# Kernel optimization log

Measured on AMD Instinct MI355X. Metric: run time of the kernel, lower is better.

Reference implementation:

```python
import jax, jax.numpy as jnp
import numpy as np

EPS = 1e-6

def _det3(m):
    return (m[..., 0, 0] * m[..., 1, 1] * m[..., 2, 2]
            + m[..., 0, 1] * m[..., 1, 2] * m[..., 2, 0]
            + m[..., 1, 0] * m[..., 2, 1] * m[..., 0, 2]
            - m[..., 2, 0] * m[..., 1, 1] * m[..., 0, 2]
            - m[..., 0, 0] * m[..., 2, 1] * m[..., 1, 2]
            - m[..., 1, 0] * m[..., 0, 1] * m[..., 2, 2])

def _inv3(m):
    a, b, c = m[..., 0, 0], m[..., 0, 1], m[..., 0, 2]
    d, e, f = m[..., 1, 0], m[..., 1, 1], m[..., 1, 2]
    g, h, i = m[..., 2, 0], m[..., 2, 1], m[..., 2, 2]
    adj = jnp.stack([
        jnp.stack([e * i - f * h, c * h - b * i, b * f - c * e], -1),
        jnp.stack([f * g - d * i, a * i - c * g, c * d - a * f], -1),
        jnp.stack([d * h - e * g, b * g - a * h, a * e - b * d], -1)], -2)
    return adj / _det3(m)[..., None, None]

def setup_inputs() -> dict:
    key = jax.random.key(0)
    ks = jax.random.split(key, 12)
    N, B, DH = 100000, 2048, 256
    idx = jnp.sort(jnp.concatenate([jnp.arange(B, dtype=jnp.int32),
                                    jax.random.randint(ks[0], (N - B,), 0, B, dtype=jnp.int32)]))
    return {
        "t": jax.random.uniform(ks[1], (B, 1), jnp.float32, 0.01, 0.99),
        "h": jax.random.normal(ks[2], (N, DH), jnp.float32),
        "pos": jax.random.normal(ks[3], (N, 3), jnp.float32),
        "eps_h": jax.random.normal(ks[4], (N, DH), jnp.float32),
        "eps_pos": jax.random.normal(ks[5], (N, 3), jnp.float32),
        "gparam_h": jax.random.normal(ks[6], (1, 1), jnp.float32),
        "gparam_pos": jax.random.normal(ks[7], (1, 1), jnp.float32),
        "W_mu": jax.random.normal(ks[8], (DH, DH), jnp.float32) / np.sqrt(DH),
        "W_r1": jax.random.normal(ks[9], (DH, 2 * DH), jnp.float32) / np.sqrt(DH),
        "W_r2": jax.random.normal(ks[10], (2 * DH, DH), jnp.float32) / np.sqrt(2 * DH),
        "index": idx,
        "num_graphs": B,
    }


def _forward(t, h, pos, eps_h, eps_pos, gparam_h, gparam_pos, W_mu, W_r1, W_r2, index, B):
    eye = jnp.eye(3, dtype=h.dtype)
    seg_sum = lambda x: jax.ops.segment_sum(x, index, num_segments=B)
    counts = seg_sum(jnp.ones((index.shape[0],), h.dtype))  # [B]

    def scatter_center(x):  # x - per-graph mean, gathered back
        mean = seg_sum(x) / counts[:, None]
        return x - mean[index]

    # volatility g(t): per-graph, gathered to nodes
    g_h = (0.1 + jax.nn.softplus(gparam_h) * t)[index]      # [N,1]
    g_pos = (0.1 + jax.nn.softplus(gparam_pos) * t)[index]  # [N,1]

    def f_net(t_, hh, pp):  # surrogate forward transformation f
        tn = t_[index]                                      # [N,1]
        mu_h = (hh @ W_mu) * (1.0 - tn)
        sigma_h = 0.1 + 0.9 * tn                            # [N,1]
        mu_pos = pp * (1.0 - tn)
        nrm = pp / (jnp.linalg.norm(pp, axis=-1, keepdims=True) + EPS)
        a = (0.2 + 0.8 * tn)[..., None]                     # [N,1,1]
        b = (0.1 * tn)[..., None]
        U = a * eye + b * (nrm[:, :, None] * nrm[:, None, :])  # [N,3,3]
        return mu_h, sigma_h, mu_pos, U

    def z_pos_fn(mu, U, eps):
        return mu + scatter_center(jnp.einsum('nij,nj->ni', U, eps))

    def score_pos_fn(eps, U, inv_U=None, C=None):
        if inv_U is None or C is None:
            inv_U = _inv3(U)
            inv_V = _inv3(seg_sum(inv_U))
            C = inv_V[index] @ (inv_U - eye)
        y = jnp.einsum('nji,nj->ni', inv_U, eps)
        ybar = seg_sum(y)
        c = jnp.einsum('nji,nj->ni', C, ybar[index])
        return scatter_center(c - y)  # zero_cog_score=True

    def solve_pos_fn(U, prel):
        inv_U = _inv3(U)
        inv_V = _inv3(seg_sum(inv_U))
        C = inv_V[index] @ (inv_U - eye)
        c = seg_sum(jnp.einsum('nij,nj->ni', C, prel))[index]
        eps = jnp.einsum('nij,nj->ni', inv_U, prel - c)
        return eps, inv_U, C

    bdrift = lambda dz, score, g: dz - 0.5 * g ** 2 * score

    # ---- target backward drift (time_derivative via jvp over t) ----
    (mu_h, sig_h, mu_p, U), (dmu_h, dsig_h, dmu_p, dU) = jax.jvp(
        lambda tt: f_net(tt, h, pos), (t,), (jnp.ones_like(t),))
    z_h = mu_h + sig_h * eps_h
    dz_h = dmu_h + dsig_h * eps_h
    z_p = z_pos_fn(mu_p, U, eps_pos)
    dz_p = z_pos_fn(dmu_p, dU, eps_pos)
    tgt_h = bdrift(dz_h, -eps_h / sig_h, g_h)
    tgt_p = bdrift(dz_p, score_pos_fn(eps_pos, U), g_pos)

    # ---- approximate backward drift ('x0' parameterization) ----
    h_r = jnp.tanh(z_h @ W_r1) @ W_r2   # reconstructor r
    pos_r = z_p * 0.9
    (mu_h2, sig_h2, mu_p2, U2), (dmu_h2, dsig_h2, dmu_p2, dU2) = jax.jvp(
        lambda tt: f_net(tt, h_r, pos_r), (t,), (jnp.ones_like(t),))
    eps_h2 = (z_h - mu_h2) / sig_h2
    eps_p2, inv_U2, C2 = solve_pos_fn(U2, z_p - mu_p2)
    dz_h2 = dmu_h2 + dsig_h2 * eps_h2
    dz_p2 = z_pos_fn(dmu_p2, dU2, eps_p2)
    apx_h = bdrift(dz_h2, -eps_h2 / sig_h2, g_h)
    apx_p = bdrift(dz_p2, score_pos_fn(eps_p2, U2, inv_U2, C2), g_pos)

    # ---- 'simple' loss: mse(approx/g, target/g) ----
    loss_h = jnp.mean(((apx_h - tgt_h) / g_h) ** 2)
    loss_p = jnp.mean(((apx_p - tgt_p) / g_pos) ** 2)
    return loss_h, loss_p


def reference(t, h, pos, eps_h, eps_pos, gparam_h, gparam_pos, W_mu, W_r1, W_r2, index, num_graphs):
    return _forward(t, h, pos, eps_h, eps_pos, gparam_h, gparam_pos, W_mu, W_r1, W_r2, index, num_graphs)
```

## Files before the change

kernel.cpp:

```cpp
#include <hip/hip_runtime.h>
#include <math.h>

#define NTHREADS 256
#define EPSC 1e-6f
#define NPL 3

typedef short bf16x8 __attribute__((ext_vector_type(8)));
typedef float f32x4  __attribute__((ext_vector_type(4)));

#define GLDS(srcp, dstp) __builtin_amdgcn_global_load_lds( \
    (const __attribute__((address_space(1))) void*)(srcp), \
    (__attribute__((address_space(3))) void*)(dstp), 16, 0, 0)

__device__ __forceinline__ ushort f2bf(float x) {
  union { float f; unsigned u; } v; v.f = x;
  unsigned r = v.u + 0x7FFFu + ((v.u >> 16) & 1u);
  return (ushort)(r >> 16);
}
__device__ __forceinline__ float bf2f(ushort x) {
  union { unsigned u; float f; } v; v.u = ((unsigned)x) << 16;
  return v.f;
}
__device__ __forceinline__ float tanh_fast(float x) {
  float xc = fminf(fmaxf(x, -15.f), 15.f);
  float e = __expf(2.f * xc);
  return (e - 1.f) / (e + 1.f);
}

__device__ __forceinline__ void inv3x3(const float m[9], float o[9]) {
  float a=m[0],b=m[1],c=m[2],d=m[3],e=m[4],f=m[5],g=m[6],h=m[7],i=m[8];
  float det = a*e*i + b*f*g + d*h*c - g*e*c - a*h*f - d*b*i;
  float r = 1.0f/det;
  o[0]=(e*i-f*h)*r; o[1]=(c*h-b*i)*r; o[2]=(b*f-c*e)*r;
  o[3]=(f*g-d*i)*r; o[4]=(a*i-c*g)*r; o[5]=(c*d-a*f)*r;
  o[6]=(d*h-e*g)*r; o[7]=(b*g-a*h)*r; o[8]=(a*e-b*d)*r;
}

__device__ __forceinline__ float wred(float v) {
#pragma unroll
  for (int o = 32; o > 0; o >>= 1) v += __shfl_xor(v, o, 64);
  return v;
}

__device__ void pos_graph(
    int b, int lane, int N,
    const float* __restrict__ pos, const float* __restrict__ epsp,
    const int* __restrict__ index, const float* __restrict__ t,
    const float* __restrict__ gpp, double* __restrict__ lossp)
{
  int lo = 0, hi = N;
  while (lo < hi) { int mid = (lo + hi) >> 1; if (index[mid] < b) lo = mid + 1; else hi = mid; }
  const int start = lo;
  hi = N;
  while (lo < hi) { int mid = (lo + hi) >> 1; if (index[mid] < b + 1) lo = mid + 1; else hi = mid; }
  const int end = lo;
  const int cnt = end - start;
  const float fn = (float)cnt, rc = 1.0f / fn;

  const float tn  = t[b];
  const float a1  = 0.2f + 0.8f*tn, b1 = 0.1f*tn;
  const float omt = 1.0f - tn;
  const float sp  = log1pf(expf(gpp[0]));
  const float gp  = 0.1f + sp*tn;
  const float hg  = 0.5f*gp*gp;
  const float rgp = 1.0f/gp;
  const float pscale = 1.0f - 0.9f*omt;

  float iU[NPL][9], yv[NPL][3], wv[NPL][3], dwv[NPL][3], pv[NPL][3];
  float Vs[9] = {0}, wb[3] = {0}, dwb[3] = {0}, yb[3] = {0};
#pragma unroll
  for (int k = 0; k < NPL; ++k) {
    const int n = start + k*64 + lane;
    if (n < end) {
      const float px = pos[3*(size_t)n+0], py = pos[3*(size_t)n+1], pz = pos[3*(size_t)n+2];
      const float ex = epsp[3*(size_t)n+0], ey = epsp[3*(size_t)n+1], ez = epsp[3*(size_t)n+2];
      pv[k][0]=px; pv[k][1]=py; pv[k][2]=pz;
      const float pn = sqrtf(px*px+py*py+pz*pz) + EPSC;
      const float nx = px/pn, ny = py/pn, nz = pz/pn;
      const float nd = nx*ex + ny*ey + nz*ez;
      wv[k][0]=a1*ex + b1*nd*nx; wv[k][1]=a1*ey + b1*nd*ny; wv[k][2]=a1*ez + b1*nd*nz;
      dwv[k][0]=0.8f*ex + 0.1f*nd*nx; dwv[k][1]=0.8f*ey + 0.1f*nd*ny; dwv[k][2]=0.8f*ez + 0.1f*nd*nz;
      const float U[9] = { a1 + b1*nx*nx, b1*nx*ny,      b1*nx*nz,
                           b1*ny*nx,      a1 + b1*ny*ny, b1*ny*nz,
                           b1*nz*nx,      b1*nz*ny,      a1 + b1*nz*nz };
      inv3x3(U, iU[k]);
      yv[k][0] = iU[k][0]*ex + iU[k][3]*ey + iU[k][6]*ez;
      yv[k][1] = iU[k][1]*ex + iU[k][4]*ey + iU[k][7]*ez;
      yv[k][2] = iU[k][2]*ex + iU[k][5]*ey + iU[k][8]*ez;
#pragma unroll
      for (int j = 0; j < 9; ++j) Vs[j] += iU[k][j];
#pragma unroll
      for (int j = 0; j < 3; ++j) { wb[j]+=wv[k][j]; dwb[j]+=dwv[k][j]; yb[j]+=yv[k][j]; }
    }
  }
#pragma unroll
  for (int j = 0; j < 9; ++j) Vs[j] = wred(Vs[j]);
#pragma unroll
  for (int j = 0; j < 3; ++j) { wb[j]=wred(wb[j]); dwb[j]=wred(dwb[j]); yb[j]=wred(yb[j]); }

  float iV[9]; inv3x3(Vs, iV);
  float wm[3], dwm[3], u1[3], s1m[3];
#pragma unroll
  for (int i = 0; i < 3; ++i) { wm[i] = wb[i]*rc; dwm[i] = dwb[i]*rc; }
#pragma unroll
  for (int i = 0; i < 3; ++i) u1[i] = iV[0*3+i]*yb[0] + iV[1*3+i]*yb[1] + iV[2*3+i]*yb[2];
#pragma unroll
  for (int i = 0; i < 3; ++i) {
    const float csy = Vs[0*3+i]*u1[0] + Vs[1*3+i]*u1[1] + Vs[2*3+i]*u1[2] - fn*u1[i];
    s1m[i] = (csy - yb[i]) * rc;
  }

  float tg[NPL][3], zp[NPL][3], iU2[NPL][9], qv[NPL][3];
  float Vs2[9] = {0}, qs[3] = {0}, ps[3] = {0};
#pragma unroll
  for (int k = 0; k < NPL; ++k) {
    const int n = start + k*64 + lane;
    if (n < end) {
#pragma unroll
      for (int i = 0; i < 3; ++i) {
        const float c1 = iU[k][0*3+i]*u1[0] + iU[k][1*3+i]*u1[1] + iU[k][2*3+i]*u1[2] - u1[i];
        const float score1 = c1 - yv[k][i] - s1m[i];
        tg[k][i] = -pv[k][i] + dwv[k][i] - dwm[i] - hg*score1;
        zp[k][i] = pv[k][i]*omt + wv[k][i] - wm[i];
      }
      const float rx = 0.9f*zp[k][0], ry = 0.9f*zp[k][1], rz = 0.9f*zp[k][2];
      const float rn = sqrtf(rx*rx+ry*ry+rz*rz) + EPSC;
      const float nx = rx/rn, ny = ry/rn, nz = rz/rn;
      const float U2[9] = { a1 + b1*nx*nx, b1*nx*ny,      b1*nx*nz,
                            b1*ny*nx,      a1 + b1*ny*ny, b1*ny*nz,
                            b1*nz*nx,      b1*nz*ny,      a1 + b1*nz*nz };
      inv3x3(U2, iU2[k]);
      float prel[3];
#pragma unroll
      for (int i = 0; i < 3; ++i) prel[i] = zp[k][i]*pscale;
#pragma unroll
      for (int i = 0; i < 3; ++i)
        qv[k][i] = iU2[k][i*3+0]*prel[0] + iU2[k][i*3+1]*prel[1] + iU2[k][i*3+2]*prel[2];
#pragma unroll
      for (int j = 0; j < 9; ++j) Vs2[j] += iU2[k][j];
#pragma unroll
      for (int j = 0; j < 3; ++j) { qs[j] += qv[k][j]; ps[j] += prel[j]; }
    }
  }
#pragma unroll
  for (int j = 0; j < 9; ++j) Vs2[j] = wred(Vs2[j]);
#pragma unroll
  for (int j = 0; j < 3; ++j) { qs[j] = wred(qs[j]); ps[j] = wred(ps[j]); }

  float iV2[9]; inv3x3(Vs2, iV2);
  float cb2[3];
#pragma unroll
  for (int i = 0; i < 3; ++i)
    cb2[i] = iV2[i*3+0]*(qs[0]-ps[0]) + iV2[i*3+1]*(qs[1]-ps[1]) + iV2[i*3+2]*(qs[2]-ps[2]);

  float y2v[NPL][3], dw2v[NPL][3];
  float yb2[3] = {0}, dwb2[3] = {0};
#pragma unroll
  for (int k = 0; k < NPL; ++k) {
    const int n = start + k*64 + lane;
    if (n < end) {
      float e[3];
#pragma unroll
      for (int i = 0; i < 3; ++i)
        e[i] = qv[k][i] - (iU2[k][i*3+0]*cb2[0] + iU2[k][i*3+1]*cb2[1] + iU2[k][i*3+2]*cb2[2]);
#pragma unroll
      for (int i = 0; i < 3; ++i)
        y2v[k][i] = iU2[k][0*3+i]*e[0] + iU2[k][1*3+i]*e[1] + iU2[k][2*3+i]*e[2];
      const float rx = 0.9f*zp[k][0], ry = 0.9f*zp[k][1], rz = 0.9f*zp[k][2];
      const float rn = sqrtf(rx*rx+ry*ry+rz*rz) + EPSC;
      const float nx = rx/rn, ny = ry/rn, nz = rz/rn;
      const float nd = nx*e[0] + ny*e[1] + nz*e[2];
      dw2v[k][0] = 0.8f*e[0] + 0.1f*nd*nx;
      dw2v[k][1] = 0.8f*e[1] + 0.1f*nd*ny;
      dw2v[k][2] = 0.8f*e[2] + 0.1f*nd*nz;
#pragma unroll
      for (int j = 0; j < 3; ++j) { yb2[j] += y2v[k][j]; dwb2[j] += dw2v[k][j]; }
    }
  }
#pragma unroll
  for (int j = 0; j < 3; ++j) { yb2[j] = wred(yb2[j]); dwb2[j] = wred(dwb2[j]); }

  float u2[3], s2m[3], dw2m[3];
#pragma unroll
  for (int i = 0; i < 3; ++i) u2[i] = iV2[0*3+i]*yb2[0] + iV2[1*3+i]*yb2[1] + iV2[2*3+i]*yb2[2];
#pragma unroll
  for (int i = 0; i < 3; ++i) {
    const float csy = Vs2[0*3+i]*u2[0] + Vs2[1*3+i]*u2[1] + Vs2[2*3+i]*u2[2] - fn*u2[i];
    s2m[i] = (csy - yb2[i]) * rc;
    dw2m[i] = dwb2[i] * rc;
  }

  float acc = 0.0f;
#pragma unroll
  for (int k = 0; k < NPL; ++k) {
    const int n = start + k*64 + lane;
    if (n < end) {
#pragma unroll
      for (int i = 0; i < 3; ++i) {
        const float c2 = iU2[k][0*3+i]*u2[0] + iU2[k][1*3+i]*u2[1] + iU2[k][2*3+i]*u2[2] - u2[i];
        const float score2 = c2 - y2v[k][i] - s2m[i];
        const float dz2 = -0.9f*zp[k][i] + dw2v[k][i] - dw2m[i];
        const float apx = dz2 - hg*score2;
        const float d = (apx - tg[k][i]) * rgp;
        acc += d*d;
      }
    }
  }
  acc = wred(acc);
  if (lane == 0) atomicAdd(lossp, (double)acc);
}

__global__ __launch_bounds__(NTHREADS) void prep_all(
    const float4* __restrict__ h, ushort4* __restrict__ hb, int n4h,
    const float4* __restrict__ wr2, ushort4* __restrict__ wr2b, int n4w,
    const float* __restrict__ wmu, ushort* __restrict__ wmut,
    const float* __restrict__ wr1, ushort* __restrict__ wr1t)
{
  __shared__ float ts[32][33];
  const int bid = blockIdx.x;
  if (bid < 2048) {
    for (int i = bid*NTHREADS + threadIdx.x; i < n4h; i += 2048*NTHREADS) {
      float4 v = h[i];
      hb[i] = make_ushort4(f2bf(v.x), f2bf(v.y), f2bf(v.z), f2bf(v.w));
    }
  } else if (bid < 2176) {
    for (int i = (bid-2048)*NTHREADS + threadIdx.x; i < n4w; i += 128*NTHREADS) {
      float4 v = wr2[i];
      wr2b[i] = make_ushort4(f2bf(v.x), f2bf(v.y), f2bf(v.z), f2bf(v.w));
    }
  } else if (bid < 2240) {
    const int vb = bid - 2176;
    const int nb = (vb & 7)*32, kb = (vb >> 3)*32;
    const int tx = threadIdx.x & 31, ty = threadIdx.x >> 5;
#pragma unroll
    for (int r = 0; r < 4; ++r)
      ts[ty + r*8][tx] = wmu[(size_t)(kb + ty + r*8)*256 + nb + tx];
    __syncthreads();
#pragma unroll
    for (int r = 0; r < 4; ++r)
      wmut[(size_t)(nb + ty + r*8)*256 + kb + tx] = f2bf(ts[tx][ty + r*8]);
  } else {
    const int vb = bid - 2240;
    const int nb = (vb & 15)*32, kb = (vb >> 4)*32;
    const int tx = threadIdx.x & 31, ty = threadIdx.x >> 5;
#pragma unroll
    for (int r = 0; r < 4; ++r)
      ts[ty + r*8][tx] = wr1[(size_t)(kb + ty + r*8)*512 + nb + tx];
    __syncthreads();
#pragma unroll
    for (int r = 0; r < 4; ++r)
      wr1t[(size_t)(nb + ty + r*8)*256 + kb + tx] = f2bf(ts[tx][ty + r*8]);
  }
}

__global__ __launch_bounds__(256) void gemm_wcomb(
    const ushort* __restrict__ A, const ushort* __restrict__ Bt,
    int K, int Nn, int Mvalid, ushort* __restrict__ OutB)
{
  __shared__ __align__(16) ushort As[128*32];
  __shared__ __align__(16) ushort Bs[128*32];
  const int tid = threadIdx.x;
  const int row0 = blockIdx.y*128, col0 = blockIdx.x*128;
  const int wave = tid >> 6, lane = tid & 63;
  const int wm = (wave & 1)*64, wn = (wave >> 1)*64;
  const int lm = lane & 15, lq = lane >> 4;

  f32x4 acc[4][4];
#pragma unroll
  for (int i = 0; i < 4; ++i)
#pragma unroll
    for (int j = 0; j < 4; ++j) { acc[i][j][0]=0.f; acc[i][j][1]=0.f; acc[i][j][2]=0.f; acc[i][j][3]=0.f; }

  const int c0 = tid, c1 = tid + 256;
  const int r0a = c0 >> 2, k0a = (c0 & 3) << 3;
  const int r1a = c1 >> 2, k1a = (c1 & 3) << 3;

  for (int k0 = 0; k0 < K; k0 += 32) {
    __syncthreads();
    GLDS(A  + (size_t)(row0 + r0a)*K + k0 + k0a, As + c0*8);
    GLDS(A  + (size_t)(row0 + r1a)*K + k0 + k1a, As + c1*8);
    GLDS(Bt + (size_t)(col0 + r0a)*K + k0 + k0a, Bs + c0*8);
    GLDS(Bt + (size_t)(col0 + r1a)*K + k0 + k1a, Bs + c1*8);
    __syncthreads();

    bf16x8 af[4], bfr[4];
#pragma unroll
    for (int i = 0; i < 4; ++i)
      af[i] = *(const bf16x8*)&As[(wm + i*16 + lm)*32 + lq*8];
#pragma unroll
    for (int j = 0; j < 4; ++j)
      bfr[j] = *(const bf16x8*)&Bs[(wn + j*16 + lm)*32 + lq*8];
#pragma unroll
    for (int i = 0; i < 4; ++i)
#pragma unroll
      for (int j = 0; j < 4; ++j)
        acc[i][j] = __builtin_amdgcn_mfma_f32_16x16x32_bf16(af[i], bfr[j], acc[i][j], 0, 0, 0);
  }

#pragma unroll
  for (int i = 0; i < 4; ++i) {
#pragma unroll
    for (int reg = 0; reg < 4; ++reg) {
      const int r = row0 + wm + i*16 + lq*4 + reg;
#pragma unroll
      for (int j = 0; j < 4; ++j) {
        const int cc = col0 + wn + j*16 + lm;
        OutB[(size_t)cc*Mvalid + r] = f2bf(-acc[i][j][reg]);
      }
    }
  }
}

__global__ __launch_bounds__(256, 3) void fused_main(
    int PB, int Bg,
    const float* __restrict__ pos, const float* __restrict__ epsp,
    const float* __restrict__ gpp, double* __restrict__ lossp,
    const ushort* __restrict__ hb, const ushort* __restrict__ wmut,
    const ushort* __restrict__ wr1t, const ushort* __restrict__ wct,
    const float* __restrict__ eps, const int* __restrict__ index,
    const float* __restrict__ t, const float* __restrict__ gph,
    int N, double* __restrict__ lossAcc)
{
  __shared__ __align__(16) ushort zs[64*256];
  __shared__ __align__(16) ushort t1s[64*128];

  const int wave = threadIdx.x >> 6, lane = threadIdx.x & 63;

  if (blockIdx.x < PB) {
    const int b = blockIdx.x*4 + wave;
    if (b < Bg) pos_graph(b, lane, N, pos, epsp, index, t, gpp, lossp);
    return;
  }

  const int row0 = (blockIdx.x - PB) * 64;
  const int lm = lane & 15, lq = lane >> 4;
  const int wn  = wave * 64;
  const int wn2 = wave * 32;

  f32x4 acc[4][4];
#pragma unroll
  for (int i = 0; i < 4; ++i)
#pragma unroll
    for (int j = 0; j < 4; ++j) { acc[i][j][0]=0.f; acc[i][j][1]=0.f; acc[i][j][2]=0.f; acc[i][j][3]=0.f; }

#pragma unroll
  for (int k = 0; k < 8; ++k) {
    bf16x8 a_[4], b_[4];
#pragma unroll
    for (int i = 0; i < 4; ++i)
      a_[i] = *(const bf16x8*)(hb + (size_t)(row0 + i*16 + lm)*256 + k*32 + lq*8);
#pragma unroll
    for (int j = 0; j < 4; ++j)
      b_[j] = *(const bf16x8*)(wmut + (size_t)(wn + j*16 + lm)*256 + k*32 + lq*8);
#pragma unroll
    for (int i = 0; i < 4; ++i)
#pragma unroll
      for (int j = 0; j < 4; ++j)
        acc[i][j] = __builtin_amdgcn_mfma_f32_16x16x32_bf16(a_[i], b_[j], acc[i][j], 0, 0, 0);
  }

#pragma unroll
  for (int i = 0; i < 4; ++i) {
#pragma unroll
    for (int reg = 0; reg < 4; ++reg) {
      const int rb = i*16 + lq*4 + reg;
      const int r = row0 + rb;
      const int rcl = (r < N) ? r : (N - 1);
      const float tn = t[index[rcl]];
      const float s0 = 1.0f - tn, s1 = 0.1f + 0.9f*tn;
#pragma unroll
      for (int j = 0; j < 4; ++j) {
        const int cc = wn + j*16 + lm;
        const float z = acc[i][j][reg]*s0 + s1*eps[(size_t)rcl*256 + cc];
        zs[rb*256 + (cc ^ ((rb & 7) << 3))] = f2bf(z);
      }
    }
  }
  __syncthreads();

  for (int c2 = 0; c2 < 4; ++c2) {
    f32x4 acct[4][2];
#pragma unroll
    for (int i = 0; i < 4; ++i)
#pragma unroll
      for (int j = 0; j < 2; ++j) { acct[i][j][0]=0.f; acct[i][j][1]=0.f; acct[i][j][2]=0.f; acct[i][j][3]=0.f; }

#pragma unroll
    for (int k = 0; k < 8; ++k) {
      bf16x8 az[4], b_[2];
#pragma unroll
      for (int i = 0; i < 4; ++i) {
        const int r = i*16 + lm;
        const int c = k*32 + lq*8;
        az[i] = *(const bf16x8*)&zs[r*256 + (c ^ ((r & 7) << 3))];
      }
#pragma unroll
      for (int j = 0; j < 2; ++j)
        b_[j] = *(const bf16x8*)(wr1t + (size_t)(c2*128 + wn2 + j*16 + lm)*256 + k*32 + lq*8);
#pragma unroll
      for (int i = 0; i < 4; ++i)
#pragma unroll
        for (int j = 0; j < 2; ++j)
          acct[i][j] = __builtin_amdgcn_mfma_f32_16x16x32_bf16(az[i], b_[j], acct[i][j], 0, 0, 0);
    }

    bf16x8 pb[4];
#pragma unroll
    for (int j = 0; j < 4; ++j)
      pb[j] = *(const bf16x8*)(wct + (size_t)(wn + j*16 + lm)*512 + c2*128 + lq*8);

    __syncthreads();
#pragma unroll
    for (int i = 0; i < 4; ++i)
#pragma unroll
      for (int j = 0; j < 2; ++j)
#pragma unroll
        for (int reg = 0; reg < 4; ++reg) {
          const int rb = i*16 + lq*4 + reg;
          const int c = wn2 + j*16 + lm;
          t1s[rb*128 + (c ^ ((rb & 7) << 3))] = f2bf(tanh_fast(acct[i][j][reg]));
        }
    __syncthreads();

#pragma unroll
    for (int k = 0; k < 4; ++k) {
      bf16x8 at[4], b_[4];
#pragma unroll
      for (int i = 0; i < 4; ++i) {
        const int r = i*16 + lm;
        const int c = k*32 + lq*8;
        at[i] = *(const bf16x8*)&t1s[r*128 + (c ^ ((r & 7) << 3))];
      }
      if (k == 0) {
#pragma unroll
        for (int j = 0; j < 4; ++j) b_[j] = pb[j];
      } else {
#pragma unroll
        for (int j = 0; j < 4; ++j)
          b_[j] = *(const bf16x8*)(wct + (size_t)(wn + j*16 + lm)*512 + c2*128 + k*32 + lq*8);
      }
#pragma unroll
      for (int i = 0; i < 4; ++i)
#pragma unroll
        for (int j = 0; j < 4; ++j)
          acc[i][j] = __builtin_amdgcn_mfma_f32_16x16x32_bf16(at[i], b_[j], acc[i][j], 0, 0, 0);
    }
  }

  const float sp = log1pf(expf(gph[0]));
  float local = 0.f;
#pragma unroll
  for (int i = 0; i < 4; ++i) {
#pragma unroll
    for (int reg = 0; reg < 4; ++reg) {
      const int r = row0 + i*16 + lq*4 + reg;
      if (r < N) {
        const float tn = t[index[r]];
        const float gh  = 0.1f + sp*tn;
        const float sig = 0.1f + 0.9f*tn;
        const float fac = 1.0f + (0.9f + 0.5f*gh*gh/sig)*(1.0f - tn)/sig;
        const float sc  = fac/gh;
#pragma unroll
        for (int j = 0; j < 4; ++j) {
          const float d = acc[i][j][reg] * sc;
          local += d*d;
        }
      }
    }
  }
  double dv = (double)local;
#pragma unroll
  for (int off = 32; off > 0; off >>= 1) dv += __shfl_down(dv, off, 64);
  if (lane == 0) atomicAdd(lossAcc, dv);
}

__global__ void finalize_kernel(const double* lossh, const double* lossp,
                                float* out, int N, int DH)
{
  if (threadIdx.x == 0) {
    out[0] = (float)(lossh[0] / ((double)N * (double)DH));
    out[1] = (float)(lossp[0] / ((double)N * 3.0));
  }
}

extern "C" void kernel_launch(void* const* d_in, const int* in_sizes, int n_in,
                              void* d_out, int out_size, void* d_ws, size_t ws_size,
                              hipStream_t stream) {
  const float* t      = (const float*)d_in[0];
  const float* h      = (const float*)d_in[1];
  const float* pos    = (const float*)d_in[2];
  const float* eps_h  = (const float*)d_in[3];
  const float* eps_p  = (const float*)d_in[4];
  const float* gph    = (const float*)d_in[5];
  const float* gpp    = (const float*)d_in[6];
  const float* W_mu   = (const float*)d_in[7];
  const float* W_r1   = (const float*)d_in[8];
  const float* W_r2   = (const float*)d_in[9];
  const int*   index  = (const int*)d_in[10];
  const int B = in_sizes[0];
  const int N = in_sizes[10];
  const int DH = 256, DH2 = 512;
  const int NPAD = 100352;

  char* ws = (char*)d_ws;
  size_t off = 0;
  auto alloc = [&](size_t nbytes) { size_t o = off; off += (nbytes + 255) & ~(size_t)255; return o; };

  size_t o_loss = alloc(16);
  size_t o_hb   = alloc((size_t)NPAD*DH*2);
  size_t o_wmut = alloc((size_t)DH*DH*2);
  size_t o_wr1t = alloc((size_t)DH2*DH*2);
  size_t o_wr2b = alloc((size_t)DH2*DH*2);
  size_t o_wct  = alloc((size_t)DH*DH2*2);

  hipMemsetAsync(ws + o_loss, 0, 16, stream);

  double* lossh = (double*)(ws + o_loss);
  double* lossp = lossh + 1;
  ushort* hb   = (ushort*)(ws + o_hb);
  ushort* wmut = (ushort*)(ws + o_wmut);
  ushort* wr1t = (ushort*)(ws + o_wr1t);
  ushort* wr2b = (ushort*)(ws + o_wr2b);
  ushort* wct  = (ushort*)(ws + o_wct);

  prep_all<<<2368, NTHREADS, 0, stream>>>(
      (const float4*)h, (ushort4*)hb, N*DH/4,
      (const float4*)W_r2, (ushort4*)wr2b, DH2*DH/4,
      W_mu, wmut, W_r1, wr1t);

  gemm_wcomb<<<dim3(DH/128, DH2/128), 256, 0, stream>>>(
      wr2b, wmut, DH, DH, DH2, wct);

  const int PB = (B + 3) / 4;
  const int HB = (N + 63) / 64;
  fused_main<<<PB + HB, 256, 0, stream>>>(
      PB, B, pos, eps_p, gpp, lossp,
      hb, wmut, wr1t, wct, eps_h, index, t, gph, N, lossh);

  finalize_kernel<<<1, 64, 0, stream>>>(lossh, lossp, (float*)d_out, N, DH);
}
```

Baseline: 545.5 us.

## Fuse h bf16 conversion into main GEMM and split pos branch into own kernel

Drops the separate pass that converted all of h to a bf16 workspace copy. The main h kernel now reads fp32 h directly and packs it to bf16 in registers before the MFMA, which removes a full write and re-read of the converted matrix. The per-graph position branch moves out of the fused kernel into its own launch with one 64-thread block per graph. The h kernel's occupancy hint drops from 3 to 2 blocks per CU and the wct prefetch is removed, trading a bigger fp32 load per tile for less total memory traffic.

Result: faster. 489.2 us (-10.3%).

```diff
diff --git a/kernel.cpp b/kernel.cpp
--- a/kernel.cpp
+++ b/kernel.cpp
@@ -20,6 +20,12 @@
 __device__ __forceinline__ float bf2f(ushort x) {
   union { unsigned u; float f; } v; v.u = ((unsigned)x) << 16;
   return v.f;
+}
+__device__ __forceinline__ bf16x8 pack8(float4 a, float4 b) {
+  bf16x8 r;
+  r[0]=(short)f2bf(a.x); r[1]=(short)f2bf(a.y); r[2]=(short)f2bf(a.z); r[3]=(short)f2bf(a.w);
+  r[4]=(short)f2bf(b.x); r[5]=(short)f2bf(b.y); r[6]=(short)f2bf(b.z); r[7]=(short)f2bf(b.w);
+  return r;
 }
 __device__ __forceinline__ float tanh_fast(float x) {
   float xc = fminf(fmaxf(x, -15.f), 15.f);
@@ -42,12 +48,14 @@
   return v;
 }
 
-__device__ void pos_graph(
-    int b, int lane, int N,
-    const float* __restrict__ pos, const float* __restrict__ epsp,
+__global__ __launch_bounds__(64) void pos_branch_v4b(
+    int N, const float* __restrict__ pos, const float* __restrict__ epsp,
     const int* __restrict__ index, const float* __restrict__ t,
     const float* __restrict__ gpp, double* __restrict__ lossp)
 {
+  const int b = blockIdx.x;
+  const int lane = threadIdx.x;
+
   int lo = 0, hi = N;
   while (lo < hi) { int mid = (lo + hi) >> 1; if (index[mid] < b) lo = mid + 1; else hi = mid; }
   const int start = lo;
@@ -210,26 +218,21 @@
   if (lane == 0) atomicAdd(lossp, (double)acc);
 }
 
-__global__ __launch_bounds__(NTHREADS) void prep_all(
-    const float4* __restrict__ h, ushort4* __restrict__ hb, int n4h,
+__global__ __launch_bounds__(NTHREADS) void prep_weights_v4b(
     const float4* __restrict__ wr2, ushort4* __restrict__ wr2b, int n4w,
     const float* __restrict__ wmu, ushort* __restrict__ wmut,
     const float* __restrict__ wr1, ushort* __restrict__ wr1t)
 {
   __shared__ float ts[32][33];
   const int bid = blockIdx.x;
-  if (bid < 2048) {
-    for (int i = bid*NTHREADS + threadIdx.x; i < n4h; i += 2048*NTHREADS) {
-      float4 v = h[i];
-      hb[i] = make_ushort4(f2bf(v.x), f2bf(v.y), f2bf(v.z), f2bf(v.w));
-    }
-  } else if (bid < 2176) {
-    for (int i = (bid-2048)*NTHREADS + threadIdx.x; i < n4w; i += 128*NTHREADS) {
+  if (bid < 128) {
+    const int i = bid*NTHREADS + threadIdx.x;
+    if (i < n4w) {
       float4 v = wr2[i];
       wr2b[i] = make_ushort4(f2bf(v.x), f2bf(v.y), f2bf(v.z), f2bf(v.w));
     }
-  } else if (bid < 2240) {
-    const int vb = bid - 2176;
+  } else if (bid < 192) {
+    const int vb = bid - 128;
     const int nb = (vb & 7)*32, kb = (vb >> 3)*32;
     const int tx = threadIdx.x & 31, ty = threadIdx.x >> 5;
 #pragma unroll
@@ -240,7 +243,7 @@
     for (int r = 0; r < 4; ++r)
       wmut[(size_t)(nb + ty + r*8)*256 + kb + tx] = f2bf(ts[tx][ty + r*8]);
   } else {
-    const int vb = bid - 2240;
+    const int vb = bid - 192;
     const int nb = (vb & 15)*32, kb = (vb >> 4)*32;
     const int tx = threadIdx.x & 31, ty = threadIdx.x >> 5;
 #pragma unroll
@@ -253,7 +256,7 @@
   }
 }
 
-__global__ __launch_bounds__(256) void gemm_wcomb(
+__global__ __launch_bounds__(256) void wcomb_gemm_v4b(
     const ushort* __restrict__ A, const ushort* __restrict__ Bt,
     int K, int Nn, int Mvalid, ushort* __restrict__ OutB)
 {
@@ -311,11 +314,8 @@
   }
 }
 
-__global__ __launch_bounds__(256, 3) void fused_main(
-    int PB, int Bg,
-    const float* __restrict__ pos, const float* __restrict__ epsp,
-    const float* __restrict__ gpp, double* __restrict__ lossp,
-    const ushort* __restrict__ hb, const ushort* __restrict__ wmut,
+__global__ __launch_bounds__(256, 2) void h_branch_v4b(
+    const float* __restrict__ hf, const ushort* __restrict__ wmut,
     const ushort* __restrict__ wr1t, const ushort* __restrict__ wct,
     const float* __restrict__ eps, const int* __restrict__ index,
     const float* __restrict__ t, const float* __restrict__ gph,
@@ -325,14 +325,7 @@
   __shared__ __align__(16) ushort t1s[64*128];
 
   const int wave = threadIdx.x >> 6, lane = threadIdx.x & 63;
-
-  if (blockIdx.x < PB) {
-    const int b = blockIdx.x*4 + wave;
-    if (b < Bg) pos_graph(b, lane, N, pos, epsp, index, t, gpp, lossp);
-    return;
-  }
-
-  const int row0 = (blockIdx.x - PB) * 64;
+  const int row0 = blockIdx.x * 64;
   const int lm = lane & 15, lq = lane >> 4;
   const int wn  = wave * 64;
   const int wn2 = wave * 32;
@@ -347,8 +340,11 @@
   for (int k = 0; k < 8; ++k) {
     bf16x8 a_[4], b_[4];
 #pragma unroll
-    for (int i = 0; i < 4; ++i)
-      a_[i] = *(const bf16x8*)(hb + (size_t)(row0 + i*16 + lm)*256 + k*32 + lq*8);
+    for (int i = 0; i < 4; ++i) {
+      int r = row0 + i*16 + lm; if (r >= N) r = N - 1;
+      const float4* p = (const float4*)(hf + (size_t)r*256 + k*32 + lq*8);
+      a_[i] = pack8(p[0], p[1]);
+    }
 #pragma unroll
     for (int j = 0; j < 4; ++j)
       b_[j] = *(const bf16x8*)(wmut + (size_t)(wn + j*16 + lm)*256 + k*32 + lq*8);
@@ -404,11 +400,6 @@
           acct[i][j] = __builtin_amdgcn_mfma_f32_16x16x32_bf16(az[i], b_[j], acct[i][j], 0, 0, 0);
     }
 
-    bf16x8 pb[4];
-#pragma unroll
-    for (int j = 0; j < 4; ++j)
-      pb[j] = *(const bf16x8*)(wct + (size_t)(wn + j*16 + lm)*512 + c2*128 + lq*8);
-
     __syncthreads();
 #pragma unroll
     for (int i = 0; i < 4; ++i)
@@ -431,14 +422,9 @@
         const int c = k*32 + lq*8;
         at[i] = *(const bf16x8*)&t1s[r*128 + (c ^ ((r & 7) << 3))];
       }
-      if (k == 0) {
-#pragma unroll
-        for (int j = 0; j < 4; ++j) b_[j] = pb[j];
-      } else {
-#pragma unroll
-        for (int j = 0; j < 4; ++j)
-          b_[j] = *(const bf16x8*)(wct + (size_t)(wn + j*16 + lm)*512 + c2*128 + k*32 + lq*8);
-      }
+#pragma unroll
+      for (int j = 0; j < 4; ++j)
+        b_[j] = *(const bf16x8*)(wct + (size_t)(wn + j*16 + lm)*512 + c2*128 + k*32 + lq*8);
 #pragma unroll
       for (int i = 0; i < 4; ++i)
 #pragma unroll
@@ -474,8 +460,8 @@
   if (lane == 0) atomicAdd(lossAcc, dv);
 }
 
-__global__ void finalize_kernel(const double* lossh, const double* lossp,
-                                float* out, int N, int DH)
+__global__ void finalize_v4b(const double* lossh, const double* lossp,
+                             float* out, int N, int DH)
 {
   if (threadIdx.x == 0) {
     out[0] = (float)(lossh[0] / ((double)N * (double)DH));
@@ -500,14 +486,12 @@
   const int B = in_sizes[0];
   const int N = in_sizes[10];
   const int DH = 256, DH2 = 512;
-  const int NPAD = 100352;
 
   char* ws = (char*)d_ws;
   size_t off = 0;
   auto alloc = [&](size_t nbytes) { size_t o = off; off += (nbytes + 255) & ~(size_t)255; return o; };
 
   size_t o_loss = alloc(16);
-  size_t o_hb   = alloc((size_t)NPAD*DH*2);
   size_t o_wmut = alloc((size_t)DH*DH*2);
   size_t o_wr1t = alloc((size_t)DH2*DH*2);
   size_t o_wr2b = alloc((size_t)DH2*DH*2);
@@ -517,25 +501,23 @@
 
   double* lossh = (double*)(ws + o_loss);
   double* lossp = lossh + 1;
-  ushort* hb   = (ushort*)(ws + o_hb);
   ushort* wmut = (ushort*)(ws + o_wmut);
   ushort* wr1t = (ushort*)(ws + o_wr1t);
   ushort* wr2b = (ushort*)(ws + o_wr2b);
   ushort* wct  = (ushort*)(ws + o_wct);
 
-  prep_all<<<2368, NTHREADS, 0, stream>>>(
-      (const float4*)h, (ushort4*)hb, N*DH/4,
+  pos_branch_v4b<<<B, 64, 0, stream>>>(N, pos, eps_p, index, t, gpp, lossp);
+
+  prep_weights_v4b<<<320, NTHREADS, 0, stream>>>(
       (const float4*)W_r2, (ushort4*)wr2b, DH2*DH/4,
       W_mu, wmut, W_r1, wr1t);
 
-  gemm_wcomb<<<dim3(DH/128, DH2/128), 256, 0, stream>>>(
+  wcomb_gemm_v4b<<<dim3(DH/128, DH2/128), 256, 0, stream>>>(
       wr2b, wmut, DH, DH, DH2, wct);
 
-  const int PB = (B + 3) / 4;
   const int HB = (N + 63) / 64;
-  fused_main<<<PB + HB, 256, 0, stream>>>(
-      PB, B, pos, eps_p, gpp, lossp,
-      hb, wmut, wr1t, wct, eps_h, index, t, gph, N, lossh);
-
-  finalize_kernel<<<1, 64, 0, stream>>>(lossh, lossp, (float*)d_out, N, DH);
-}
+  h_branch_v4b<<<HB, 256, 0, stream>>>(
+      h, wmut, wr1t, wct, eps_h, index, t, gph, N, lossh);
+
+  finalize_v4b<<<1, 64, 0, stream>>>(lossh, lossp, (float*)d_out, N, DH);
+}
```
